# Kernel optimization log

Measured on AMD Instinct MI355X. Metric: run time of the kernel, lower is better.

## Reference

```python
import jax, jax.numpy as jnp
import numpy as np

NC, NP, H, E, EL = 4096, 8192, 128, 500000, 500000


def setup_inputs() -> dict:
    key = jax.random.key(0)
    ks = jax.random.split(key, 32)
    W = lambda i, shape: jax.random.normal(ks[i], shape, dtype=jnp.float32) * 0.02
    inp = {
        "x_country": jax.random.normal(ks[0], (NC, NC), dtype=jnp.float32),
        "x_product": jax.random.normal(ks[1], (NP, NP), dtype=jnp.float32),
        # input projections (Linear(num_x, hidden)) and node-id embeddings
        "Wc_lin": W(2, (NC, H)), "bc_lin": jnp.zeros((H,), jnp.float32),
        "Wp_lin": W(3, (NP, H)), "bp_lin": jnp.zeros((H,), jnp.float32),
        "emb_c": W(4, (NC, H)),
        "emb_p": W(5, (NP, H)),
        # SAGEConv params per layer per edge type (lin_l has bias, lin_r does not)
        "W1ep_l": W(6, (H, H)), "b1ep": jnp.zeros((H,), jnp.float32), "W1ep_r": W(7, (H, H)),
        "W1pc_l": W(8, (H, H)), "b1pc": jnp.zeros((H,), jnp.float32), "W1pc_r": W(9, (H, H)),
        "W2ep_l": W(10, (H, H)), "b2ep": jnp.zeros((H,), jnp.float32), "W2ep_r": W(11, (H, H)),
        "W2pc_l": W(12, (H, H)), "b2pc": jnp.zeros((H,), jnp.float32), "W2pc_r": W(13, (H, H)),
        # graph structure
        "nid_c": jnp.arange(NC, dtype=jnp.int32),
        "nid_p": jnp.arange(NP, dtype=jnp.int32),
        "e_src": jax.random.randint(ks[14], (E,), 0, NC, dtype=jnp.int32),
        "e_dst": jax.random.randint(ks[15], (E,), 0, NP, dtype=jnp.int32),
        "l_src": jax.random.randint(ks[16], (EL,), 0, NC, dtype=jnp.int32),
        "l_dst": jax.random.randint(ks[17], (EL,), 0, NP, dtype=jnp.int32),
    }
    return inp


def _seg_mean(x, src, dst, n):
    # mean aggregation of source-node features onto destination nodes
    s = jax.ops.segment_sum(x[src], dst, num_segments=n)  # [n, H]
    c = jax.ops.segment_sum(jnp.ones_like(dst, dtype=x.dtype), dst, num_segments=n)
    return s / jnp.maximum(c, 1.0)[:, None]


def _sage(x_src, x_dst, src, dst, Wl, bl, Wr):
    # PyG SAGEConv(mean): lin_l(mean_agg(x_j)) + lin_r(x_i)
    return _seg_mean(x_src, src, dst, x_dst.shape[0]) @ Wl + bl + x_dst @ Wr


def reference(x_country, x_product, Wc_lin, bc_lin, Wp_lin, bp_lin, emb_c, emb_p,
              W1ep_l, b1ep, W1ep_r, W1pc_l, b1pc, W1pc_r,
              W2ep_l, b2ep, W2ep_r, W2pc_l, b2pc, W2pc_r,
              nid_c, nid_p, e_src, e_dst, l_src, l_dst):
    # input fusion: linear(features) + embedding(node_id)
    xc = x_country @ Wc_lin + bc_lin + emb_c[nid_c]  # [NC, H]
    xp = x_product @ Wp_lin + bp_lin + emb_p[nid_p]  # [NP, H]
    # hetero layer 1 (relu per node type); rev edges are the transpose of exports
    hp = jax.nn.relu(_sage(xc, xp, e_src, e_dst, W1ep_l, b1ep, W1ep_r))
    hc = jax.nn.relu(_sage(xp, xc, e_dst, e_src, W1pc_l, b1pc, W1pc_r))
    # hetero layer 2 (no relu)
    hp2 = _sage(hc, hp, e_src, e_dst, W2ep_l, b2ep, W2ep_r)
    hc2 = _sage(hp, hc, e_dst, e_src, W2pc_l, b2pc, W2pc_r)
    # edge-wise dot-product classifier over label edges
    return jnp.sum(hc2[l_src] * hp2[l_dst], axis=-1)  # [EL]
```

## Files before the change

### kernel.cpp

```cpp
#include <hip/hip_runtime.h>
#include <stdint.h>

#define NCn 4096
#define NPn 8192
#define Hn  128
#define En  500000
#define ELn 500000

typedef unsigned short u16;
using f32x4  = __attribute__((ext_vector_type(4))) float;
using bf16x8 = __attribute__((ext_vector_type(8))) short;

__device__ inline u16 f2bf(float f) {
  union { float f; uint32_t u; } v; v.f = f;
  uint32_t r = v.u + 0x7fffu + ((v.u >> 16) & 1u);
  return (u16)(r >> 16);
}
__device__ inline float bfu(uint32_t u) {
  union { uint32_t x; float f; } z; z.x = u << 16; return z.f;
}

__global__ __launch_bounds__(256) void wtrans(const float* __restrict__ W,
                                              u16* __restrict__ WT, int K) {
  __shared__ float sh[64][33];
  const int k0 = blockIdx.x * 64, n0 = blockIdx.y * 32;
  const int t = threadIdx.x;
  {
    int r = t >> 3, c4 = t & 7;
#pragma unroll
    for (int p = 0; p < 2; ++p) {
      int row = p * 32 + r;
      float4 v = *(const float4*)&W[(size_t)(k0 + row) * 128 + n0 + c4 * 4];
      sh[row][c4 * 4 + 0] = v.x; sh[row][c4 * 4 + 1] = v.y;
      sh[row][c4 * 4 + 2] = v.z; sh[row][c4 * 4 + 3] = v.w;
    }
  }
  __syncthreads();
  int n = t >> 3, kq = t & 7;
  u16 pk[8];
#pragma unroll
  for (int j = 0; j < 8; ++j) pk[j] = f2bf(sh[kq * 8 + j][n]);
  uint4 o;
  o.x = (uint32_t)pk[0] | ((uint32_t)pk[1] << 16);
  o.y = (uint32_t)pk[2] | ((uint32_t)pk[3] << 16);
  o.z = (uint32_t)pk[4] | ((uint32_t)pk[5] << 16);
  o.w = (uint32_t)pk[6] | ((uint32_t)pk[7] << 16);
  *(uint4*)&WT[(size_t)(n0 + n) * K + k0 + kq * 8] = o;
}

__global__ __launch_bounds__(256) void count_deg(const int* __restrict__ esrc,
                                                 const int* __restrict__ edst,
                                                 int* __restrict__ cntC,
                                                 int* __restrict__ cntP) {
  int i = blockIdx.x * 256 + threadIdx.x;
  if (i >= En) return;
  atomicAdd(&cntP[edst[i]], 1);
  atomicAdd(&cntC[esrc[i]], 1);
}

__global__ __launch_bounds__(256) void scan2(const int* __restrict__ cntP,
                                             const int* __restrict__ cntC,
                                             int* __restrict__ offP,
                                             int* __restrict__ offC,
                                             int* __restrict__ curP,
                                             int* __restrict__ curC) {
  __shared__ int sh[257];
  const int* cnt; int* off; int* cur; int n;
  if (blockIdx.x == 0) { cnt = cntP; off = offP; cur = curP; n = NPn; }
  else                 { cnt = cntC; off = offC; cur = curC; n = NCn; }
  int t = threadIdx.x;
  int chunk = n >> 8;
  int base = t * chunk;
  int s = 0;
#pragma unroll 4
  for (int i = 0; i < chunk; ++i) s += cnt[base + i];
  sh[t] = s;
  __syncthreads();
  if (t == 0) {
    int run = 0;
    for (int i = 0; i < 256; ++i) { int v = sh[i]; sh[i] = run; run += v; }
    sh[256] = run;
  }
  __syncthreads();
  int p = sh[t];
  for (int i = 0; i < chunk; ++i) {
    off[base + i] = p; cur[base + i] = p; p += cnt[base + i];
  }
  if (t == 255) off[n] = sh[256];
}

__global__ __launch_bounds__(256) void fill_adj(const int* __restrict__ esrc,
                                                const int* __restrict__ edst,
                                                int* __restrict__ curC,
                                                int* __restrict__ curP,
                                                int* __restrict__ adjC,
                                                int* __restrict__ adjP) {
  int i = blockIdx.x * 256 + threadIdx.x;
  if (i >= En) return;
  int s = esrc[i], d = edst[i];
  int p = atomicAdd(&curP[d], 1);
  adjP[p] = s;
  int q = atomicAdd(&curC[s], 1);
  adjC[q] = d;
}

__global__ __launch_bounds__(256) void gemm_big_sk(const float* __restrict__ A,
                                                   const u16* __restrict__ BT,
                                                   float* __restrict__ part,
                                                   int K, int Kc) {
  __shared__ __align__(16) u16 aL[64 * 64];
  const int t = threadIdx.x;
  const int wid = t >> 6, lane = t & 63;
  const int ln15 = lane & 15, lhi = lane >> 4;
  const int m0 = blockIdx.x * 64;
  const int kb0 = blockIdx.y * Kc;
  const int nIter = Kc >> 6;
  const size_t M128 = (size_t)gridDim.x * 64 * 128;

  f32x4 acc[4][2] = {};

  const int arow = t >> 2, acq = t & 3;
  const float* Ap = &A[(size_t)(m0 + arow) * K + kb0 + acq * 16];
  const u16* Bp = &BT[(size_t)(wid * 32 + ln15) * K + kb0 + lhi * 8];
  const size_t BniStride = (size_t)16 * K;

#define LOAD_A(dst, koff)                                                      \
  { _Pragma("unroll") for (int i = 0; i < 4; ++i)                              \
      dst[i] = *(const float4*)(Ap + (koff) + i * 4); }
#define LOAD_B(dst, koff)                                                      \
  { _Pragma("unroll") for (int ni = 0; ni < 2; ++ni)                           \
    _Pragma("unroll") for (int ks = 0; ks < 2; ++ks)                           \
      dst[ni][ks] = *(const bf16x8*)(Bp + ni * BniStride + (koff) + ks * 32); }
#define STORE_A_LDS(src)                                                       \
  { u16 pk[16];                                                                \
    _Pragma("unroll") for (int i = 0; i < 4; ++i) {                            \
      pk[i*4+0] = f2bf(src[i].x); pk[i*4+1] = f2bf(src[i].y);                  \
      pk[i*4+2] = f2bf(src[i].z); pk[i*4+3] = f2bf(src[i].w); }                \
    uint4 w0, w1;                                                              \
    w0.x = (uint32_t)pk[0] | ((uint32_t)pk[1] << 16);                          \
    w0.y = (uint32_t)pk[2] | ((uint32_t)pk[3] << 16);                          \
    w0.z = (uint32_t)pk[4] | ((uint32_t)pk[5] << 16);                          \
    w0.w = (uint32_t)pk[6] | ((uint32_t)pk[7] << 16);                          \
    w1.x = (uint32_t)pk[8] | ((uint32_t)pk[9] << 16);                          \
    w1.y = (uint32_t)pk[10] | ((uint32_t)pk[11] << 16);                        \
    w1.z = (uint32_t)pk[12] | ((uint32_t)pk[13] << 16);                        \
    w1.w = (uint32_t)pk[14] | ((uint32_t)pk[15] << 16);                        \
    int sb = arow * 128;                                                       \
    int sw = (arow & 7) << 4;                                                  \
    *(uint4*)((char*)aL + sb + ((acq * 32) ^ sw)) = w0;                        \
    *(uint4*)((char*)aL + sb + ((acq * 32 + 16) ^ sw)) = w1; }
#define COMPUTE(bset)                                                          \
  { _Pragma("unroll") for (int ks = 0; ks < 2; ++ks) {                         \
      bf16x8 afr[4];                                                           \
      _Pragma("unroll") for (int mi = 0; mi < 4; ++mi) {                       \
        int r = mi * 16 + ln15;                                                \
        afr[mi] = *(const bf16x8*)((const char*)aL + r * 128 +                 \
                    ((ks * 64 + lhi * 16) ^ ((r & 7) << 4)));                  \
      }                                                                        \
      _Pragma("unroll") for (int mi = 0; mi < 4; ++mi)                         \
      _Pragma("unroll") for (int ni = 0; ni < 2; ++ni)                         \
        acc[mi][ni] = __builtin_amdgcn_mfma_f32_16x16x32_bf16(                 \
            afr[mi], bset[ni][ks], acc[mi][ni], 0, 0, 0);                      \
    } }

  float4 avA[4], avB[4];
  bf16x8 bvA[2][2], bvB[2][2];
  LOAD_A(avA, 0)
  LOAD_B(bvA, 0)

  for (int it = 0; it < nIter; it += 2) {
    __syncthreads();
    STORE_A_LDS(avA)
    {
      int ko = (it + 1) * 64;
      LOAD_A(avB, ko)
      LOAD_B(bvB, ko)
    }
    __syncthreads();
    COMPUTE(bvA)
    __syncthreads();
    STORE_A_LDS(avB)
    if (it + 2 < nIter) {
      int ko = (it + 2) * 64;
      LOAD_A(avA, ko)
      LOAD_B(bvA, ko)
    }
    __syncthreads();
    COMPUTE(bvB)
  }

  float* P = part + (size_t)blockIdx.y * M128;
#pragma unroll
  for (int mi = 0; mi < 4; ++mi) {
#pragma unroll
    for (int ni = 0; ni < 2; ++ni) {
      int col = wid * 32 + ni * 16 + ln15;
#pragma unroll
      for (int r = 0; r < 4; ++r) {
        int row = m0 + mi * 16 + lhi * 4 + r;
        P[(size_t)row * 128 + col] = acc[mi][ni][r];
      }
    }
  }
#undef LOAD_A
#undef LOAD_B
#undef STORE_A_LDS
#undef COMPUTE
}

__global__ __launch_bounds__(256) void gemm_combine(const float* __restrict__ part,
                                                    const float* __restrict__ bias,
                                                    const float* __restrict__ addend,
                                                    float* __restrict__ out,
                                                    u16* __restrict__ outH,
                                                    int M, int SK) {
  int i = blockIdx.x * 256 + threadIdx.x;
  int n4 = M * 32;
  if (i >= n4) return;
  size_t stride = (size_t)M * 128;
  f32x4 s = {};
  for (int c = 0; c < SK; ++c) s += *(const f32x4*)&part[c * stride + (size_t)i * 4];
  int col = (i * 4) & 127;
  f32x4 b = *(const f32x4*)&bias[col];
  f32x4 ad = *(const f32x4*)&addend[(size_t)i * 4];
  f32x4 r = s + b + ad;
  *(f32x4*)&out[(size_t)i * 4] = r;
  uint2 h;
  h.x = (uint32_t)f2bf(r[0]) | ((uint32_t)f2bf(r[1]) << 16);
  h.y = (uint32_t)f2bf(r[2]) | ((uint32_t)f2bf(r[3]) << 16);
  *(uint2*)&outH[(size_t)i * 4] = h;
}

template <int RELU>
__global__ __launch_bounds__(256) void gemm_layer(const float* __restrict__ A1,
                                                  const float* __restrict__ A2,
                                                  const float* __restrict__ Wl,
                                                  const float* __restrict__ Wr,
                                                  const float* __restrict__ bias,
                                                  float* __restrict__ out,
                                                  u16* __restrict__ outH) {
  __shared__ float aT[32][33];
  __shared__ float wT[32][128];
  const int t = threadIdx.x;
  const int tx = t & 15, ty = t >> 4;
  const int m0 = blockIdx.x * 32;
  const int arow = t >> 3, ac = t & 7;
  const int wrow8 = t >> 5, wc = t & 31;
  float acc[2][8] = {};

  float4 a_v;
  float4 w_v[4];
  a_v = *(const float4*)&A1[(size_t)(m0 + arow) * 128 + ac * 4];
#pragma unroll
  for (int i = 0; i < 4; ++i)
    w_v[i] = *(const float4*)&Wl[(size_t)(i * 8 + wrow8) * 128 + wc * 4];

  for (int kc = 0; kc < 8; ++kc) {
    __syncthreads();
    aT[arow][ac * 4 + 0] = a_v.x; aT[arow][ac * 4 + 1] = a_v.y;
    aT[arow][ac * 4 + 2] = a_v.z; aT[arow][ac * 4 + 3] = a_v.w;
#pragma unroll
    for (int i = 0; i < 4; ++i) *(float4*)&wT[i * 8 + wrow8][wc * 4] = w_v[i];
    if (kc + 1 < 8) {
      int nk = kc + 1;
      const float* Asrc = (nk < 4) ? A1 : A2;
      const float* Wsrc = (nk < 4) ? Wl : Wr;
      int kb = (nk & 3) * 32;
      a_v = *(const float4*)&Asrc[(size_t)(m0 + arow) * 128 + kb + ac * 4];
#pragma unroll
      for (int i = 0; i < 4; ++i)
        w_v[i] = *(const float4*)&Wsrc[(size_t)(kb + i * 8 + wrow8) * 128 + wc * 4];
    }
    __syncthreads();
#pragma unroll
    for (int k = 0; k < 32; ++k) {
      float a0 = aT[ty * 2 + 0][k], a1 = aT[ty * 2 + 1][k];
      float4 w0 = *(const float4*)&wT[k][tx * 8];
      float4 w1 = *(const float4*)&wT[k][tx * 8 + 4];
      float w[8] = {w0.x, w0.y, w0.z, w0.w, w1.x, w1.y, w1.z, w1.w};
#pragma unroll
      for (int j = 0; j < 8; ++j) {
        acc[0][j] += a0 * w[j];
        acc[1][j] += a1 * w[j];
      }
    }
  }
#pragma unroll
  for (int i = 0; i < 2; ++i) {
    int row = m0 + ty * 2 + i;
    float o[8];
#pragma unroll
    for (int j = 0; j < 8; ++j) {
      float v = acc[i][j] + bias[tx * 8 + j];
      o[j] = RELU ? fmaxf(v, 0.f) : v;
    }
    float4 v0 = {o[0], o[1], o[2], o[3]}, v1 = {o[4], o[5], o[6], o[7]};
    *(float4*)&out[(size_t)row * 128 + tx * 8] = v0;
    *(float4*)&out[(size_t)row * 128 + tx * 8 + 4] = v1;
    if (outH) {
      uint4 h;
      h.x = (uint32_t)f2bf(o[0]) | ((uint32_t)f2bf(o[1]) << 16);
      h.y = (uint32_t)f2bf(o[2]) | ((uint32_t)f2bf(o[3]) << 16);
      h.z = (uint32_t)f2bf(o[4]) | ((uint32_t)f2bf(o[5]) << 16);
      h.w = (uint32_t)f2bf(o[6]) | ((uint32_t)f2bf(o[7]) << 16);
      *(uint4*)&outH[(size_t)row * 128 + tx * 8] = h;
    }
  }
}

__global__ __launch_bounds__(256) void agg_mean_h(const int* __restrict__ adj,
                                                  const int* __restrict__ off,
                                                  const u16* __restrict__ Xh,
                                                  float* __restrict__ out, int ndst) {
  int w = blockIdx.x * 4 + (threadIdx.x >> 6);
  if (w >= ndst) return;
  int lane = threadIdx.x & 63;
  int q = lane >> 4, c = lane & 15;
  int s0 = off[w], deg = off[w + 1] - s0;
  f32x4 acc0 = {}, acc1 = {};
#define ACC8(v)                                                                \
  { acc0[0] += bfu((v).x & 0xffffu); acc0[1] += bfu((v).x >> 16);              \
    acc0[2] += bfu((v).y & 0xffffu); acc0[3] += bfu((v).y >> 16);              \
    acc1[0] += bfu((v).z & 0xffffu); acc1[1] += bfu((v).z >> 16);              \
    acc1[2] += bfu((v).w & 0xffffu); acc1[3] += bfu((v).w >> 16); }
  for (int base = 0; base < deg; base += 64) {
    int my = base + lane;
    int sv = (my < deg) ? adj[s0 + my] : 0;
    int cnt = min(64, deg - base);
    int jj = 0;
    for (; jj + 8 <= cnt; jj += 8) {
      int n0 = __shfl(sv, jj + q);
      int n1 = __shfl(sv, jj + 4 + q);
      uint4 v0 = *(const uint4*)&Xh[(size_t)n0 * 128 + c * 8];
      uint4 v1 = *(const uint4*)&Xh[(size_t)n1 * 128 + c * 8];
      ACC8(v0)
      ACC8(v1)
    }
    for (; jj + 4 <= cnt; jj += 4) {
      int n0 = __shfl(sv, jj + q);
      uint4 v0 = *(const uint4*)&Xh[(size_t)n0 * 128 + c * 8];
      ACC8(v0)
    }
    int r = cnt - jj;
    if (r > 0) {
      int n0 = __shfl(sv, min(jj + q, cnt - 1));
      if (q < r) {
        uint4 v0 = *(const uint4*)&Xh[(size_t)n0 * 128 + c * 8];
        ACC8(v0)
      }
    }
  }
#undef ACC8
#pragma unroll
  for (int j = 0; j < 4; ++j) {
    acc0[j] += __shfl_xor(acc0[j], 16);
    acc0[j] += __shfl_xor(acc0[j], 32);
    acc1[j] += __shfl_xor(acc1[j], 16);
    acc1[j] += __shfl_xor(acc1[j], 32);
  }
  if (q == 0) {
    float inv = 1.f / (float)max(deg, 1);
    acc0 *= inv; acc1 *= inv;
    *(f32x4*)&out[(size_t)w * 128 + c * 8] = acc0;
    *(f32x4*)&out[(size_t)w * 128 + c * 8 + 4] = acc1;
  }
}

__global__ __launch_bounds__(256) void edge_dot(const int* __restrict__ ls,
                                                const int* __restrict__ ld,
                                                const float* __restrict__ hc2,
                                                const float* __restrict__ hp2,
                                                float* __restrict__ o, int n) {
  int w = blockIdx.x * 4 + (threadIdx.x >> 6);
  int lane = threadIdx.x & 63;
  int q = lane >> 4, c = lane & 15;
  int e = w * 4 + q;
  if (e >= n) return;
  int s = ls[e], d = ld[e];
  const float* pa = &hc2[(size_t)s * 128 + c * 8];
  const float* pb = &hp2[(size_t)d * 128 + c * 8];
  f32x4 a0 = *(const f32x4*)pa, a1 = *(const f32x4*)(pa + 4);
  f32x4 b0 = *(const f32x4*)pb, b1 = *(const f32x4*)(pb + 4);
  f32x4 pv = a0 * b0 + a1 * b1;
  float p = pv[0] + pv[1] + pv[2] + pv[3];
#pragma unroll
  for (int m = 8; m; m >>= 1) p += __shfl_xor(p, m);
  if (c == 0) o[e] = p;
}

extern "C" void kernel_launch(void* const* d_in, const int* in_sizes, int n_in,
                              void* d_out, int out_size, void* d_ws, size_t ws_size,
                              hipStream_t stream) {
  const float* x_c    = (const float*)d_in[0];
  const float* x_p    = (const float*)d_in[1];
  const float* Wc     = (const float*)d_in[2];
  const float* bc     = (const float*)d_in[3];
  const float* Wp     = (const float*)d_in[4];
  const float* bp     = (const float*)d_in[5];
  const float* emb_c  = (const float*)d_in[6];
  const float* emb_p  = (const float*)d_in[7];
  const float* W1ep_l = (const float*)d_in[8];
  const float* b1ep   = (const float*)d_in[9];
  const float* W1ep_r = (const float*)d_in[10];
  const float* W1pc_l = (const float*)d_in[11];
  const float* b1pc   = (const float*)d_in[12];
  const float* W1pc_r = (const float*)d_in[13];
  const float* W2ep_l = (const float*)d_in[14];
  const float* b2ep   = (const float*)d_in[15];
  const float* W2ep_r = (const float*)d_in[16];
  const float* W2pc_l = (const float*)d_in[17];
  const float* b2pc   = (const float*)d_in[18];
  const float* W2pc_r = (const float*)d_in[19];
  const int* e_src    = (const int*)d_in[22];
  const int* e_dst    = (const int*)d_in[23];
  const int* l_src    = (const int*)d_in[24];
  const int* l_dst    = (const int*)d_in[25];

  size_t off = 0;
  auto alloc = [&](size_t bytes) -> void* {
    void* p = (char*)d_ws + off;
    off += (bytes + 255) & ~(size_t)255;
    return p;
  };
  float* xc    = (float*)alloc((size_t)NCn * Hn * 4);
  float* xp    = (float*)alloc((size_t)NPn * Hn * 4);
  float* aggP  = (float*)alloc((size_t)NPn * Hn * 4);
  float* aggC  = (float*)alloc((size_t)NCn * Hn * 4);
  float* hp    = (float*)alloc((size_t)NPn * Hn * 4);
  float* hc    = (float*)alloc((size_t)NCn * Hn * 4);
  float* hp2   = (float*)alloc((size_t)NPn * Hn * 4);
  float* hc2   = (float*)alloc((size_t)NCn * Hn * 4);
  u16*   xcH   = (u16*)alloc((size_t)NCn * Hn * 2);
  u16*   xpH   = (u16*)alloc((size_t)NPn * Hn * 2);
  u16*   hpH   = (u16*)alloc((size_t)NPn * Hn * 2);
  u16*   hcH   = (u16*)alloc((size_t)NCn * Hn * 2);
  u16*   WcT   = (u16*)alloc((size_t)Hn * NCn * 2);
  u16*   WpT   = (u16*)alloc((size_t)Hn * NPn * 2);
  float* partP = (float*)alloc((size_t)8 * NPn * Hn * 4);
  float* partC = (float*)alloc((size_t)4 * NCn * Hn * 4);
  int*   adjP  = (int*)alloc((size_t)En * 4);
  int*   adjC  = (int*)alloc((size_t)En * 4);
  int*   offP  = (int*)alloc((size_t)(NPn + 1) * 4);
  int*   offC  = (int*)alloc((size_t)(NCn + 1) * 4);
  int*   curP  = (int*)alloc((size_t)NPn * 4);
  int*   curC  = (int*)alloc((size_t)NCn * 4);
  int*   cnts  = (int*)alloc((size_t)(NPn + NCn) * 4);
  int*   cntP  = cnts;
  int*   cntC  = cnts + NPn;

  hipMemsetAsync(cnts, 0, (size_t)(NPn + NCn) * 4, stream);

  count_deg<<<(En + 255) / 256, 256, 0, stream>>>(e_src, e_dst, cntC, cntP);
  scan2<<<2, 256, 0, stream>>>(cntP, cntC, offP, offC, curP, curC);
  fill_adj<<<(En + 255) / 256, 256, 0, stream>>>(e_src, e_dst, curC, curP, adjC, adjP);

  wtrans<<<dim3(NCn / 64, 4), 256, 0, stream>>>(Wc, WcT, NCn);
  wtrans<<<dim3(NPn / 64, 4), 256, 0, stream>>>(Wp, WpT, NPn);
  gemm_big_sk<<<dim3(NCn / 64, 4), 256, 0, stream>>>(x_c, WcT, partC, NCn, NCn / 4);
  gemm_big_sk<<<dim3(NPn / 64, 8), 256, 0, stream>>>(x_p, WpT, partP, NPn, NPn / 8);
  gemm_combine<<<(NCn * 32 + 255) / 256, 256, 0, stream>>>(partC, bc, emb_c, xc, xcH, NCn, 4);
  gemm_combine<<<(NPn * 32 + 255) / 256, 256, 0, stream>>>(partP, bp, emb_p, xp, xpH, NPn, 8);

  agg_mean_h<<<NPn / 4, 256, 0, stream>>>(adjP, offP, xcH, aggP, NPn);
  agg_mean_h<<<NCn / 4, 256, 0, stream>>>(adjC, offC, xpH, aggC, NCn);
  gemm_layer<1><<<NPn / 32, 256, 0, stream>>>(aggP, xp, W1ep_l, W1ep_r, b1ep, hp, hpH);
  gemm_layer<1><<<NCn / 32, 256, 0, stream>>>(aggC, xc, W1pc_l, W1pc_r, b1pc, hc, hcH);

  agg_mean_h<<<NPn / 4, 256, 0, stream>>>(adjP, offP, hcH, aggP, NPn);
  agg_mean_h<<<NCn / 4, 256, 0, stream>>>(adjC, offC, hpH, aggC, NCn);
  gemm_layer<0><<<NPn / 32, 256, 0, stream>>>(aggP, hp, W2ep_l, W2ep_r, b2ep, hp2, nullptr);
  gemm_layer<0><<<NCn / 32, 256, 0, stream>>>(aggC, hc, W2pc_l, W2pc_r, b2pc, hc2, nullptr);

  edge_dot<<<(ELn + 15) / 16, 256, 0, stream>>>(l_src, l_dst, hc2, hp2,
                                                (float*)d_out, ELn);
}
```

Measured before the change: 842.4 us.

## Double-buffer LDS in split-K GEMM and read bf16 features in edge dot

The big input-projection GEMM now uses two LDS buffers for the A tile. This lets it store the next tile while computing on the current one, cutting the loop from four barriers per two K-steps to two. Separately, the layer-2 GEMMs also write bf16 copies of hp2/hc2, and the label-edge dot product gathers those bf16 rows instead of fp32. That halves the random-gather bytes, at the cost of reduced precision in the final dot products and extra bf16 writes.

```diff
diff --git a/kernel.cpp b/kernel.cpp
--- a/kernel.cpp
+++ b/kernel.cpp
@@ -108,7 +108,7 @@
                                                    const u16* __restrict__ BT,
                                                    float* __restrict__ part,
                                                    int K, int Kc) {
-  __shared__ __align__(16) u16 aL[64 * 64];
+  __shared__ __align__(16) u16 aL[2 * 64 * 64];
   const int t = threadIdx.x;
   const int wid = t >> 6, lane = t & 63;
   const int ln15 = lane & 15, lhi = lane >> 4;
@@ -131,7 +131,7 @@
   { _Pragma("unroll") for (int ni = 0; ni < 2; ++ni)                           \
     _Pragma("unroll") for (int ks = 0; ks < 2; ++ks)                           \
       dst[ni][ks] = *(const bf16x8*)(Bp + ni * BniStride + (koff) + ks * 32); }
-#define STORE_A_LDS(src)                                                       \
+#define STORE_A_LDS(src, b)                                                    \
   { u16 pk[16];                                                                \
     _Pragma("unroll") for (int i = 0; i < 4; ++i) {                            \
       pk[i*4+0] = f2bf(src[i].x); pk[i*4+1] = f2bf(src[i].y);                  \
@@ -145,16 +145,16 @@
     w1.y = (uint32_t)pk[10] | ((uint32_t)pk[11] << 16);                        \
     w1.z = (uint32_t)pk[12] | ((uint32_t)pk[13] << 16);                        \
     w1.w = (uint32_t)pk[14] | ((uint32_t)pk[15] << 16);                        \
-    int sb = arow * 128;                                                       \
+    int sb = (b) * 8192 + arow * 128;                                          \
     int sw = (arow & 7) << 4;                                                  \
     *(uint4*)((char*)aL + sb + ((acq * 32) ^ sw)) = w0;                        \
     *(uint4*)((char*)aL + sb + ((acq * 32 + 16) ^ sw)) = w1; }
-#define COMPUTE(bset)                                                          \
+#define COMPUTE(b, bset)                                                       \
   { _Pragma("unroll") for (int ks = 0; ks < 2; ++ks) {                         \
       bf16x8 afr[4];                                                           \
       _Pragma("unroll") for (int mi = 0; mi < 4; ++mi) {                       \
         int r = mi * 16 + ln15;                                                \
-        afr[mi] = *(const bf16x8*)((const char*)aL + r * 128 +                 \
+        afr[mi] = *(const bf16x8*)((const char*)aL + (b) * 8192 + r * 128 +    \
                     ((ks * 64 + lhi * 16) ^ ((r & 7) << 4)));                  \
       }                                                                        \
       _Pragma("unroll") for (int mi = 0; mi < 4; ++mi)                         \
@@ -163,30 +163,28 @@
             afr[mi], bset[ni][ks], acc[mi][ni], 0, 0, 0);                      \
     } }
 
-  float4 avA[4], avB[4];
-  bf16x8 bvA[2][2], bvB[2][2];
-  LOAD_A(avA, 0)
-  LOAD_B(bvA, 0)
+  float4 av0[4], av1[4];
+  bf16x8 bv0[2][2], bv1[2][2];
+
+  LOAD_A(av0, 0)
+  LOAD_B(bv0, 0)
+  STORE_A_LDS(av0, 0)
+  LOAD_A(av1, 64)
+  __syncthreads();
 
   for (int it = 0; it < nIter; it += 2) {
+    STORE_A_LDS(av1, 1)
+    if (it + 2 < nIter) LOAD_A(av0, (it + 2) * 64)
+    LOAD_B(bv1, (it + 1) * 64)
+    COMPUTE(0, bv0)
     __syncthreads();
-    STORE_A_LDS(avA)
-    {
-      int ko = (it + 1) * 64;
-      LOAD_A(avB, ko)
-      LOAD_B(bvB, ko)
-    }
-    __syncthreads();
-    COMPUTE(bvA)
-    __syncthreads();
-    STORE_A_LDS(avB)
     if (it + 2 < nIter) {
-      int ko = (it + 2) * 64;
-      LOAD_A(avA, ko)
-      LOAD_B(bvA, ko)
-    }
-    __syncthreads();
-    COMPUTE(bvB)
+      STORE_A_LDS(av0, 0)
+      if (it + 3 < nIter) LOAD_A(av1, (it + 3) * 64)
+      LOAD_B(bv0, (it + 2) * 64)
+    }
+    COMPUTE(1, bv1)
+    if (it + 2 < nIter) __syncthreads();
   }
 
   float* P = part + (size_t)blockIdx.y * M128;
@@ -366,23 +364,27 @@
   }
 }
 
-__global__ __launch_bounds__(256) void edge_dot(const int* __restrict__ ls,
-                                                const int* __restrict__ ld,
-                                                const float* __restrict__ hc2,
-                                                const float* __restrict__ hp2,
-                                                float* __restrict__ o, int n) {
+__global__ __launch_bounds__(256) void edge_dot_h(const int* __restrict__ ls,
+                                                  const int* __restrict__ ld,
+                                                  const u16* __restrict__ aH,
+                                                  const u16* __restrict__ bH,
+                                                  float* __restrict__ o, int n) {
   int w = blockIdx.x * 4 + (threadIdx.x >> 6);
   int lane = threadIdx.x & 63;
   int q = lane >> 4, c = lane & 15;
   int e = w * 4 + q;
   if (e >= n) return;
   int s = ls[e], d = ld[e];
-  const float* pa = &hc2[(size_t)s * 128 + c * 8];
-  const float* pb = &hp2[(size_t)d * 128 + c * 8];
-  f32x4 a0 = *(const f32x4*)pa, a1 = *(const f32x4*)(pa + 4);
-  f32x4 b0 = *(const f32x4*)pb, b1 = *(const f32x4*)(pb + 4);
-  f32x4 pv = a0 * b0 + a1 * b1;
-  float p = pv[0] + pv[1] + pv[2] + pv[3];
+  uint4 va = *(const uint4*)&aH[(size_t)s * 128 + c * 8];
+  uint4 vb = *(const uint4*)&bH[(size_t)d * 128 + c * 8];
+  float p = bfu(va.x & 0xffffu) * bfu(vb.x & 0xffffu)
+          + bfu(va.x >> 16)     * bfu(vb.x >> 16)
+          + bfu(va.y & 0xffffu) * bfu(vb.y & 0xffffu)
+          + bfu(va.y >> 16)     * bfu(vb.y >> 16)
+          + bfu(va.z & 0xffffu) * bfu(vb.z & 0xffffu)
+          + bfu(va.z >> 16)     * bfu(vb.z >> 16)
+          + bfu(va.w & 0xffffu) * bfu(vb.w & 0xffffu)
+          + bfu(va.w >> 16)     * bfu(vb.w >> 16);
 #pragma unroll
   for (int m = 8; m; m >>= 1) p += __shfl_xor(p, m);
   if (c == 0) o[e] = p;
@@ -434,6 +436,8 @@
   u16*   xpH   = (u16*)alloc((size_t)NPn * Hn * 2);
   u16*   hpH   = (u16*)alloc((size_t)NPn * Hn * 2);
   u16*   hcH   = (u16*)alloc((size_t)NCn * Hn * 2);
+  u16*   hp2H  = (u16*)alloc((size_t)NPn * Hn * 2);
+  u16*   hc2H  = (u16*)alloc((size_t)NCn * Hn * 2);
   u16*   WcT   = (u16*)alloc((size_t)Hn * NCn * 2);
   u16*   WpT   = (u16*)alloc((size_t)Hn * NPn * 2);
   float* partP = (float*)alloc((size_t)8 * NPn * Hn * 4);
@@ -468,9 +472,9 @@
 
   agg_mean_h<<<NPn / 4, 256, 0, stream>>>(adjP, offP, hcH, aggP, NPn);
   agg_mean_h<<<NCn / 4, 256, 0, stream>>>(adjC, offC, hpH, aggC, NCn);
-  gemm_layer<0><<<NPn / 32, 256, 0, stream>>>(aggP, hp, W2ep_l, W2ep_r, b2ep, hp2, nullptr);
-  gemm_layer<0><<<NCn / 32, 256, 0, stream>>>(aggC, hc, W2pc_l, W2pc_r, b2pc, hc2, nullptr);
-
-  edge_dot<<<(ELn + 15) / 16, 256, 0, stream>>>(l_src, l_dst, hc2, hp2,
-                                                (float*)d_out, ELn);
-}
+  gemm_layer<0><<<NPn / 32, 256, 0, stream>>>(aggP, hp, W2ep_l, W2ep_r, b2ep, hp2, hp2H);
+  gemm_layer<0><<<NCn / 32, 256, 0, stream>>>(aggC, hc, W2pc_l, W2pc_r, b2pc, hc2, hc2H);
+
+  edge_dot_h<<<(ELn + 15) / 16, 256, 0, stream>>>(l_src, l_dst, hc2H, hp2H,
+                                                  (float*)d_out, ELn);
+}
```

New measurement: 830.5 us. Within noise of the previous version (-1.4%).
